# Optimization experiments

Measured on AMD Instinct MI355X. Metric: run time of the kernel, lower is better.

## Reference

```python
import jax, jax.numpy as jnp
import numpy as np

LEAK = 0.95
THRESHOLD = 1.0
RESCALE = 2.0


def _xavier_uniform(key, shape, gain=2.0):
    fan_out, fan_in = shape
    bound = gain * np.sqrt(6.0 / (fan_in + fan_out))
    return jax.random.uniform(key, shape, jnp.float32, -bound, bound)


def setup_inputs() -> dict:
    key = jax.random.key(0)
    k_inp, k_w1, k_w2 = jax.random.split(key, 3)
    inp = jax.random.normal(k_inp, (8192, 784), jnp.float32)
    w1 = _xavier_uniform(k_w1, (800, 784))   # fc1.weight
    w2 = _xavier_uniform(k_w2, (10, 800))    # fc2.weight
    return {"inp": inp, "w1": w1, "w2": w2, "num_steps": 25}


@jax.custom_vjp
def spike_fn(x):
    return (x > 0).astype(x.dtype)

def _spike_fwd(x):
    return spike_fn(x), x

def _spike_bwd(x, g):
    # grad = g * 0.3 * relu(1 - |x|)  (surrogate BP)
    return (g * 0.3 * jnp.maximum(1.0 - jnp.abs(x), 0.0),)

spike_fn.defvjp(_spike_fwd, _spike_bwd)


def poisson_gen(key, inp):
    r = jax.random.uniform(key, inp.shape, inp.dtype)
    temp = (r * RESCALE <= jnp.abs(inp)).astype(inp.dtype) * jnp.sign(inp)
    return 0.5 * (temp + 1.0)


def reference(inp, w1, w2, num_steps):
    batch = inp.shape[0]
    x = inp.reshape(batch, -1)
    keys = jax.random.split(jax.random.key(42), num_steps)

    def step(carry, key):
        mem1, mem2 = carry
        sp = poisson_gen(key, x)                    # [B, 784]
        mem1 = LEAK * mem1 + (1.0 - LEAK) * (sp @ w1.T)  # [B, 800]
        mem_thr = mem1 / THRESHOLD - 1.0
        out = spike_fn(mem_thr)
        rst = jnp.where(mem_thr > 0, THRESHOLD, 0.0)
        mem1 = mem1 - jax.lax.stop_gradient(rst)
        mem2 = mem2 + out @ w2.T                    # [B, 10]
        return (mem1, mem2), None

    init = (jnp.zeros((batch, 800), x.dtype), jnp.zeros((batch, 10), x.dtype))
    (_, mem2), _ = jax.lax.scan(step, init, keys)
    return mem2 / num_steps
```

## Files before the change

kernel.cpp:

```cpp
#include <hip/hip_runtime.h>
#include <cstdint>

__host__ __device__ inline uint32_t tf_rotl32(uint32_t x, uint32_t r) {
  return (x << r) | (x >> (32u - r));
}

__host__ __device__ inline void threefry2x32(uint32_t k0, uint32_t k1,
                                             uint32_t x0, uint32_t x1,
                                             uint32_t* o0, uint32_t* o1) {
  uint32_t ks0 = k0, ks1 = k1, ks2 = k0 ^ k1 ^ 0x1BD11BDAu;
  x0 += ks0; x1 += ks1;
#define TF_R(r) { x0 += x1; x1 = tf_rotl32(x1, r); x1 ^= x0; }
  TF_R(13) TF_R(15) TF_R(26) TF_R(6)
  x0 += ks1; x1 += ks2 + 1u;
  TF_R(17) TF_R(29) TF_R(16) TF_R(24)
  x0 += ks2; x1 += ks0 + 2u;
  TF_R(13) TF_R(15) TF_R(26) TF_R(6)
  x0 += ks0; x1 += ks1 + 3u;
  TF_R(17) TF_R(29) TF_R(16) TF_R(24)
  x0 += ks1; x1 += ks2 + 4u;
  TF_R(13) TF_R(15) TF_R(26) TF_R(6)
  x0 += ks2; x1 += ks0 + 5u;
#undef TF_R
  *o0 = x0; *o1 = x1;
}

#define BSZ   8192
#define KIN   784
#define HID   800
#define NOUT  10
#define NSTEP 25


__global__ __launch_bounds__(256) void enc_kernel(const float* __restrict__ inp,
                                                  uint8_t* __restrict__ enc,
                                                  uint32_t k0, uint32_t k1) {
  int j = blockIdx.x * blockDim.x + threadIdx.x;
  if (j >= BSZ * KIN) return;
  uint32_t o0, o1;
  threefry2x32(k0, k1, 0u, (uint32_t)j, &o0, &o1);
  uint32_t bits = o0 ^ o1;
  float r = __uint_as_float((bits >> 9) | 0x3f800000u) - 1.0f;
  float x = inp[j];
  bool cond = (2.0f * r <= fabsf(x));
  int s = (x > 0.0f) ? 1 : ((x < 0.0f) ? -1 : 0);
  enc[j] = (uint8_t)(1 + (cond ? s : 0));
}

#define BM 128
#define BN 32
#define BK 16

__global__ __launch_bounds__(256) void gemm_kernel(const uint8_t* __restrict__ enc,
                                                   const float* __restrict__ w1,
                                                   float* __restrict__ mem1,
                                                   uint8_t* __restrict__ spk) {
  __shared__ float As[BK * BM];
  __shared__ float Bs[BK * BN];
  const int m0 = blockIdx.x * BM;
  const int n0 = blockIdx.y * BN;
  const int t  = threadIdx.x;
  const int tn = t & 7;
  const int tm = t >> 3;
  const int arow  = t >> 1;
  const int akofs = (t & 1) * 8;
  const int brow  = t >> 3;
  const int bkofs = (t & 7) * 2;
  const int bswz  = (((brow >> 2) ^ (t & 7)) << 2) + (brow & 3);

  float acc[4][4] = {};
  float tot[4][4] = {};

#define COMMIT()                                                   \
  {                                                                \
    _Pragma("unroll") for (int mi = 0; mi < 4; mi++)               \
      _Pragma("unroll") for (int ni = 0; ni < 4; ni++) {           \
        tot[mi][ni] = __fadd_rn(tot[mi][ni], acc[mi][ni]);         \
        acc[mi][ni] = 0.0f;                                        \
      }                                                            \
  }

#define MAC_RANGE(KB, KE)                                          \
  {                                                                \
    _Pragma("unroll") for (int kk = (KB); kk < (KE); kk++) {       \
      const int q = (kk >> 1) & 7;                                 \
      float a[4], b[4];                                            \
      *(float4*)a = *(const float4*)&As[kk * BM + (tm << 2)];      \
      *(float4*)b = *(const float4*)&Bs[kk * BN + (((tn ^ q)) << 2)]; \
      _Pragma("unroll") for (int mi = 0; mi < 4; mi++)             \
        _Pragma("unroll") for (int ni = 0; ni < 4; ni++)           \
          acc[mi][ni] = fmaf(a[mi], b[ni], acc[mi][ni]);           \
    }                                                              \
  }

  int k0 = 0;
  for (int tile = 0; tile < 49; tile++, k0 += BK) {
    {
      const uint8_t* src = enc + (size_t)(m0 + arow) * KIN + k0 + akofs;
      uint2 v = *(const uint2*)src;
      As[(akofs + 0) * BM + arow] = (float)( v.x        & 0xffu);
      As[(akofs + 1) * BM + arow] = (float)((v.x >>  8) & 0xffu);
      As[(akofs + 2) * BM + arow] = (float)((v.x >> 16) & 0xffu);
      As[(akofs + 3) * BM + arow] = (float)((v.x >> 24)        );
      As[(akofs + 4) * BM + arow] = (float)( v.y        & 0xffu);
      As[(akofs + 5) * BM + arow] = (float)((v.y >>  8) & 0xffu);
      As[(akofs + 6) * BM + arow] = (float)((v.y >> 16) & 0xffu);
      As[(akofs + 7) * BM + arow] = (float)((v.y >> 24)        );
    }
    {
      const float* src = w1 + (size_t)(n0 + brow) * KIN + k0 + bkofs;
      float2 v = *(const float2*)src;
      Bs[(bkofs + 0) * BN + bswz] = v.x;
      Bs[(bkofs + 1) * BN + bswz] = v.y;
    }
    __syncthreads();
    if (tile == 16) {
      MAC_RANGE(0, 8)
      COMMIT()
      MAC_RANGE(8, 16)
    } else {
      MAC_RANGE(0, 16)
    }
    __syncthreads();
    if (tile == 32) COMMIT()
  }
  COMMIT()

#pragma unroll
  for (int mi = 0; mi < 4; mi++) {
    const size_t row = (size_t)(m0 + (tm << 2) + mi);
    float* mp = mem1 + row * HID + n0 + (tn << 2);
    float mold[4];
    *(float4*)mold = *(const float4*)mp;
    float mnew[4];
    uint32_t sbits = 0;
#pragma unroll
    for (int ni = 0; ni < 4; ni++) {
      float gv  = __fmul_rn(0.5f, tot[mi][ni]);
      float m   = __fadd_rn(__fmul_rn(0.95f, mold[ni]), __fmul_rn(0.05f, gv));
      float thr = __fadd_rn(m, -1.0f);
      bool spike = thr > 0.0f;
      mnew[ni] = spike ? thr : m;
      sbits |= (spike ? 1u : 0u) << (8 * ni);
    }
    *(float4*)mp = *(const float4*)mnew;
    *(uint32_t*)(spk + row * HID + n0 + (tn << 2)) = sbits;
  }
#undef MAC_RANGE
#undef COMMIT
}

__global__ __launch_bounds__(256) void spike_out_kernel(const uint8_t* __restrict__ spk,
                                                        const float* __restrict__ w2,
                                                        float* __restrict__ mem2) {
  __shared__ float w2s[NOUT * HID];
  for (int i = threadIdx.x; i < NOUT * HID; i += 256) w2s[i] = w2[i];
  __syncthreads();

  const int wave = threadIdx.x / 64;
  const int lane = threadIdx.x % 64;
  const int b = blockIdx.x * 4 + wave;
  const uint8_t* srow = spk + (size_t)b * HID;

  float acc[NOUT];
#pragma unroll
  for (int i = 0; i < NOUT; i++) acc[i] = 0.0f;

  for (int j = lane; j < HID; j += 64) {
    if (srow[j]) {
#pragma unroll
      for (int i = 0; i < NOUT; i++) acc[i] += w2s[i * HID + j];
    }
  }
#pragma unroll
  for (int i = 0; i < NOUT; i++) {
    float v = acc[i];
    for (int off = 32; off > 0; off >>= 1) v += __shfl_down(v, off);
    if (lane == 0) mem2[(size_t)b * NOUT + i] += v;
  }
}

__global__ __launch_bounds__(256) void finalize_kernel(const float* __restrict__ mem2,
                                                       const int* __restrict__ ns,
                                                       float* __restrict__ out) {
  int i = blockIdx.x * blockDim.x + threadIdx.x;
  if (i < BSZ * NOUT) out[i] = mem2[i] / (float)(*ns);
}

extern "C" void kernel_launch(void* const* d_in, const int* in_sizes, int n_in,
                              void* d_out, int out_size, void* d_ws, size_t ws_size,
                              hipStream_t stream) {
  const float* inp = (const float*)d_in[0];
  const float* w1  = (const float*)d_in[1];
  const float* w2  = (const float*)d_in[2];
  const int*   dns = (const int*)d_in[3];
  float* out = (float*)d_out;

  char* ws = (char*)d_ws;
  size_t off = 0;
  uint8_t* enc = (uint8_t*)(ws + off);  off += (size_t)BSZ * KIN;
  off = (off + 255) & ~(size_t)255;
  uint8_t* spk = (uint8_t*)(ws + off);  off += (size_t)BSZ * HID;
  off = (off + 255) & ~(size_t)255;
  float* mem1 = (float*)(ws + off);     off += (size_t)BSZ * HID * 4;
  float* mem2 = (float*)(ws + off);     off += (size_t)BSZ * NOUT * 4;

  (void)hipMemsetAsync(mem1, 0, (size_t)BSZ * HID * 4, stream);
  (void)hipMemsetAsync(mem2, 0, (size_t)BSZ * NOUT * 4, stream);

  uint32_t keys[NSTEP][2];
  for (int t = 0; t < NSTEP; t++)
    threefry2x32(0u, 42u, 0u, (uint32_t)t, &keys[t][0], &keys[t][1]);

  const int n_elem = BSZ * KIN;
  for (int t = 0; t < NSTEP; t++) {
    enc_kernel<<<(n_elem + 255) / 256, 256, 0, stream>>>(inp, enc, keys[t][0], keys[t][1]);
    gemm_kernel<<<dim3(BSZ / BM, HID / BN), 256, 0, stream>>>(enc, w1, mem1, spk);
    spike_out_kernel<<<BSZ / 4, 256, 0, stream>>>(spk, w2, mem2);
  }
  finalize_kernel<<<(BSZ * NOUT + 255) / 256, 256, 0, stream>>>(mem2, dns, out);
}
```

Before: 4.920 ms.

## Double K-tile depth and prefetch next tile into registers during compute

The GEMM K-tile grows from 16 to 32, so the loop runs 25 iterations instead of 49, with a guarded tail for K=784. Global loads for the next tile are issued into registers before the MAC loop so their latency overlaps computation, and loads are widened to 16-byte vectors. The partial-sum commit points move to keep the same accumulation grouping (k=256 and k=512). Shared memory use doubles and register pressure rises, which may lower occupancy.

Result: slower. 5.019 ms (+2.0%).

```diff
diff --git a/kernel.cpp b/kernel.cpp
--- a/kernel.cpp
+++ b/kernel.cpp
@@ -49,7 +49,8 @@
 
 #define BM 128
 #define BN 32
-#define BK 16
+#define BK 32
+#define NTILE 25
 
 __global__ __launch_bounds__(256) void gemm_kernel(const uint8_t* __restrict__ enc,
                                                    const float* __restrict__ w1,
@@ -62,69 +63,81 @@
   const int t  = threadIdx.x;
   const int tn = t & 7;
   const int tm = t >> 3;
-  const int arow  = t >> 1;
-  const int akofs = (t & 1) * 8;
-  const int brow  = t >> 3;
-  const int bkofs = (t & 7) * 2;
-  const int bswz  = (((brow >> 2) ^ (t & 7)) << 2) + (brow & 3);
+  const int arow = t >> 1;
+  const int ak   = (t & 1) * 16;
+  const int brow = t >> 3;
+  const int bk   = (t & 7) * 4;
+
+  const uint8_t* aptr = enc + (size_t)(m0 + arow) * KIN;
+  const float*   bptr = w1  + (size_t)(n0 + brow) * KIN;
 
   float acc[4][4] = {};
   float tot[4][4] = {};
 
-#define COMMIT()                                                   \
-  {                                                                \
-    _Pragma("unroll") for (int mi = 0; mi < 4; mi++)               \
-      _Pragma("unroll") for (int ni = 0; ni < 4; ni++) {           \
-        tot[mi][ni] = __fadd_rn(tot[mi][ni], acc[mi][ni]);         \
-        acc[mi][ni] = 0.0f;                                        \
-      }                                                            \
-  }
-
-#define MAC_RANGE(KB, KE)                                          \
-  {                                                                \
-    _Pragma("unroll") for (int kk = (KB); kk < (KE); kk++) {       \
-      const int q = (kk >> 1) & 7;                                 \
-      float a[4], b[4];                                            \
-      *(float4*)a = *(const float4*)&As[kk * BM + (tm << 2)];      \
-      *(float4*)b = *(const float4*)&Bs[kk * BN + (((tn ^ q)) << 2)]; \
-      _Pragma("unroll") for (int mi = 0; mi < 4; mi++)             \
-        _Pragma("unroll") for (int ni = 0; ni < 4; ni++)           \
-          acc[mi][ni] = fmaf(a[mi], b[ni], acc[mi][ni]);           \
-    }                                                              \
-  }
+  auto COMMIT = [&]() {
+#pragma unroll
+    for (int mi = 0; mi < 4; mi++)
+#pragma unroll
+      for (int ni = 0; ni < 4; ni++) {
+        tot[mi][ni] = __fadd_rn(tot[mi][ni], acc[mi][ni]);
+        acc[mi][ni] = 0.0f;
+      }
+  };
+
+  auto MAC = [&](int KB, int KE) {
+#pragma unroll 4
+    for (int kk = KB; kk < KE; kk++) {
+      const int q = (kk >> 1) & 7;
+      float a[4], b[4];
+      *(float4*)a = *(const float4*)&As[kk * BM + (tm << 2)];
+      *(float4*)b = *(const float4*)&Bs[kk * BN + ((tn ^ q) << 2)];
+#pragma unroll
+      for (int mi = 0; mi < 4; mi++)
+#pragma unroll
+        for (int ni = 0; ni < 4; ni++)
+          acc[mi][ni] = fmaf(a[mi], b[ni], acc[mi][ni]);
+    }
+  };
+
+  uint4  aval = *(const uint4*)(aptr + ak);
+  float4 bval = *(const float4*)(bptr + bk);
 
   int k0 = 0;
-  for (int tile = 0; tile < 49; tile++, k0 += BK) {
-    {
-      const uint8_t* src = enc + (size_t)(m0 + arow) * KIN + k0 + akofs;
-      uint2 v = *(const uint2*)src;
-      As[(akofs + 0) * BM + arow] = (float)( v.x        & 0xffu);
-      As[(akofs + 1) * BM + arow] = (float)((v.x >>  8) & 0xffu);
-      As[(akofs + 2) * BM + arow] = (float)((v.x >> 16) & 0xffu);
-      As[(akofs + 3) * BM + arow] = (float)((v.x >> 24)        );
-      As[(akofs + 4) * BM + arow] = (float)( v.y        & 0xffu);
-      As[(akofs + 5) * BM + arow] = (float)((v.y >>  8) & 0xffu);
-      As[(akofs + 6) * BM + arow] = (float)((v.y >> 16) & 0xffu);
-      As[(akofs + 7) * BM + arow] = (float)((v.y >> 24)        );
-    }
-    {
-      const float* src = w1 + (size_t)(n0 + brow) * KIN + k0 + bkofs;
-      float2 v = *(const float2*)src;
-      Bs[(bkofs + 0) * BN + bswz] = v.x;
-      Bs[(bkofs + 1) * BN + bswz] = v.y;
+  for (int tile = 0; tile < NTILE; tile++, k0 += BK) {
+    if (k0 + ak < KIN) {
+      const uint32_t w[4] = {aval.x, aval.y, aval.z, aval.w};
+#pragma unroll
+      for (int c = 0; c < 4; c++) {
+        As[(ak + 4 * c + 0) * BM + arow] = (float)( w[c]        & 0xffu);
+        As[(ak + 4 * c + 1) * BM + arow] = (float)((w[c] >>  8) & 0xffu);
+        As[(ak + 4 * c + 2) * BM + arow] = (float)((w[c] >> 16) & 0xffu);
+        As[(ak + 4 * c + 3) * BM + arow] = (float)((w[c] >> 24)        );
+      }
+    }
+    if (k0 + bk < KIN) {
+      const float f[4] = {bval.x, bval.y, bval.z, bval.w};
+#pragma unroll
+      for (int j = 0; j < 4; j++) {
+        const int k = bk + j;
+        const int q = (k >> 1) & 7;
+        Bs[k * BN + ((((brow >> 2) ^ q) << 2) | (brow & 3))] = f[j];
+      }
     }
     __syncthreads();
-    if (tile == 16) {
-      MAC_RANGE(0, 8)
-      COMMIT()
-      MAC_RANGE(8, 16)
-    } else {
-      MAC_RANGE(0, 16)
-    }
+    if (tile + 1 < NTILE) {
+      const int kn = k0 + BK;
+      const int ka = (kn + ak + 16 <= KIN) ? (kn + ak) : kn;
+      const int kb = (kn + bk + 4  <= KIN) ? (kn + bk) : kn;
+      aval = *(const uint4*)(aptr + ka);
+      bval = *(const float4*)(bptr + kb);
+    }
+    if (tile == 8)       { MAC(0, 8);  COMMIT(); MAC(8, 32); }
+    else if (tile == 16) { MAC(0, 16); COMMIT(); MAC(16, 32); }
+    else if (tile == 24) { MAC(0, 16); }
+    else                 { MAC(0, 32); }
     __syncthreads();
-    if (tile == 32) COMMIT()
-  }
-  COMMIT()
+  }
+  COMMIT();
 
 #pragma unroll
   for (int mi = 0; mi < 4; mi++) {
@@ -146,8 +159,6 @@
     *(float4*)mp = *(const float4*)mnew;
     *(uint32_t*)(spk + row * HID + n0 + (tn << 2)) = sbits;
   }
-#undef MAC_RANGE
-#undef COMMIT
 }
 
 __global__ __launch_bounds__(256) void spike_out_kernel(const uint8_t* __restrict__ spk,
```

## Double-buffer shared memory tiles and prefetch next tile in GEMM loop

Applied to the files above, without the earlier changes.

Converts the GEMM inner loop to a two-stage ping-pong shared-memory pipeline. Global loads for the next K-tile are issued into registers before the current tile's multiply-accumulate and stored to the alternate buffer afterward, leaving one barrier per tile instead of two. This is meant to hide global load latency behind compute. It doubles LDS usage and adds live registers for the prefetched values, which may lower occupancy.

Result: no change. 4.906 ms (-0.3%).

```diff
diff --git a/kernel.cpp b/kernel.cpp
--- a/kernel.cpp
+++ b/kernel.cpp
@@ -50,13 +50,14 @@
 #define BM 128
 #define BN 32
 #define BK 16
+#define NTILE 49
 
 __global__ __launch_bounds__(256) void gemm_kernel(const uint8_t* __restrict__ enc,
                                                    const float* __restrict__ w1,
                                                    float* __restrict__ mem1,
                                                    uint8_t* __restrict__ spk) {
-  __shared__ float As[BK * BM];
-  __shared__ float Bs[BK * BN];
+  __shared__ float As[2][BK * BM];
+  __shared__ float Bs[2][BK * BN];
   const int m0 = blockIdx.x * BM;
   const int n0 = blockIdx.y * BN;
   const int t  = threadIdx.x;
@@ -68,6 +69,9 @@
   const int bkofs = (t & 7) * 2;
   const int bswz  = (((brow >> 2) ^ (t & 7)) << 2) + (brow & 3);
 
+  const uint8_t* aptr = enc + (size_t)(m0 + arow) * KIN + akofs;
+  const float*   bptr = w1  + (size_t)(n0 + brow) * KIN + bkofs;
+
   float acc[4][4] = {};
   float tot[4][4] = {};
 
@@ -80,49 +84,55 @@
       }                                                            \
   }
 
-#define MAC_RANGE(KB, KE)                                          \
+#define MAC_RANGE(P, KB, KE)                                       \
   {                                                                \
     _Pragma("unroll") for (int kk = (KB); kk < (KE); kk++) {       \
       const int q = (kk >> 1) & 7;                                 \
       float a[4], b[4];                                            \
-      *(float4*)a = *(const float4*)&As[kk * BM + (tm << 2)];      \
-      *(float4*)b = *(const float4*)&Bs[kk * BN + (((tn ^ q)) << 2)]; \
+      *(float4*)a = *(const float4*)&As[P][kk * BM + (tm << 2)];   \
+      *(float4*)b = *(const float4*)&Bs[P][kk * BN + ((tn ^ q) << 2)]; \
       _Pragma("unroll") for (int mi = 0; mi < 4; mi++)             \
         _Pragma("unroll") for (int ni = 0; ni < 4; ni++)           \
           acc[mi][ni] = fmaf(a[mi], b[ni], acc[mi][ni]);           \
     }                                                              \
   }
 
-  int k0 = 0;
-  for (int tile = 0; tile < 49; tile++, k0 += BK) {
-    {
-      const uint8_t* src = enc + (size_t)(m0 + arow) * KIN + k0 + akofs;
-      uint2 v = *(const uint2*)src;
-      As[(akofs + 0) * BM + arow] = (float)( v.x        & 0xffu);
-      As[(akofs + 1) * BM + arow] = (float)((v.x >>  8) & 0xffu);
-      As[(akofs + 2) * BM + arow] = (float)((v.x >> 16) & 0xffu);
-      As[(akofs + 3) * BM + arow] = (float)((v.x >> 24)        );
-      As[(akofs + 4) * BM + arow] = (float)( v.y        & 0xffu);
-      As[(akofs + 5) * BM + arow] = (float)((v.y >>  8) & 0xffu);
-      As[(akofs + 6) * BM + arow] = (float)((v.y >> 16) & 0xffu);
-      As[(akofs + 7) * BM + arow] = (float)((v.y >> 24)        );
-    }
-    {
-      const float* src = w1 + (size_t)(n0 + brow) * KIN + k0 + bkofs;
-      float2 v = *(const float2*)src;
-      Bs[(bkofs + 0) * BN + bswz] = v.x;
-      Bs[(bkofs + 1) * BN + bswz] = v.y;
-    }
-    __syncthreads();
-    if (tile == 16) {
-      MAC_RANGE(0, 8)
-      COMMIT()
-      MAC_RANGE(8, 16)
-    } else {
-      MAC_RANGE(0, 16)
-    }
-    __syncthreads();
+#define STAGE(P, AV, BV)                                           \
+  {                                                                \
+    As[P][(akofs + 0) * BM + arow] = (float)( (AV).x        & 0xffu); \
+    As[P][(akofs + 1) * BM + arow] = (float)(((AV).x >>  8) & 0xffu); \
+    As[P][(akofs + 2) * BM + arow] = (float)(((AV).x >> 16) & 0xffu); \
+    As[P][(akofs + 3) * BM + arow] = (float)(((AV).x >> 24)        ); \
+    As[P][(akofs + 4) * BM + arow] = (float)( (AV).y        & 0xffu); \
+    As[P][(akofs + 5) * BM + arow] = (float)(((AV).y >>  8) & 0xffu); \
+    As[P][(akofs + 6) * BM + arow] = (float)(((AV).y >> 16) & 0xffu); \
+    As[P][(akofs + 7) * BM + arow] = (float)(((AV).y >> 24)        ); \
+    Bs[P][(bkofs + 0) * BN + bswz] = (BV).x;                          \
+    Bs[P][(bkofs + 1) * BN + bswz] = (BV).y;                          \
+  }
+
+  {
+    uint2  av = *(const uint2*)(aptr);
+    float2 bv = *(const float2*)(bptr);
+    STAGE(0, av, bv)
+  }
+  __syncthreads();
+
+  uint2  avn;
+  float2 bvn;
+  for (int tile = 0; tile < NTILE; tile++) {
+    const int p = tile & 1;
+    if (tile + 1 < NTILE) {
+      avn = *(const uint2*)(aptr + (tile + 1) * BK);
+      bvn = *(const float2*)(bptr + (tile + 1) * BK);
+    }
+    if (tile == 16) { MAC_RANGE(p, 0, 8) COMMIT() MAC_RANGE(p, 8, 16) }
+    else            { MAC_RANGE(p, 0, 16) }
     if (tile == 32) COMMIT()
+    if (tile + 1 < NTILE) {
+      STAGE(1 - p, avn, bvn)
+      __syncthreads();
+    }
   }
   COMMIT()
 
@@ -148,6 +158,7 @@
   }
 #undef MAC_RANGE
 #undef COMMIT
+#undef STAGE
 }
 
 __global__ __launch_bounds__(256) void spike_out_kernel(const uint8_t* __restrict__ spk,
```
